# Performance work log

Measured on AMD Instinct MI355X. Metric: run time of the kernel, lower is better.

The kernel has to match this reference:

```python
import jax, jax.numpy as jnp
import numpy as np

N, C, H, W, J = 16, 8, 512, 1024, 8


def setup_inputs() -> dict:
    key = jax.random.key(0)
    logits = jax.random.normal(key, (N, C, H, W), dtype=jnp.float32)
    rng = np.random.default_rng(0)
    start = rng.integers(0, H - 2, size=(N, J))
    length = rng.integers(1, H // 2, size=(N, J))
    end = np.minimum(start + length, H - 1)          # ensure z+1 <= H-1
    ch = rng.integers(0, C, size=(N, J))
    params = jnp.asarray(np.stack([start, end, ch], axis=-1).astype(np.int32))
    return {"logits": logits, "params": params}


def reference(logits, params):
    n, c, h, w = logits.shape
    probs = jax.nn.softmax(logits, axis=-1)
    # soft-argmax expected position over grid axis -> [n, c, h]
    pos = jnp.sum(probs * jnp.arange(w, dtype=logits.dtype), axis=-1)
    # adjacent-row position differences -> [n, c, h-1]
    diff = pos[:, :, :-1] - pos[:, :, 1:]
    start = params[..., 0]   # [n, J]
    end = params[..., 1]     # [n, J]
    ch = params[..., 2]      # [n, J]
    # gather the channel for each (sample, lane): [n, J, h-1]
    diff_g = jnp.take_along_axis(diff, ch[:, :, None].astype(jnp.int32), axis=1)
    z = jnp.arange(h - 1, dtype=jnp.int32)
    mask = (z[None, None, :] >= start[:, :, None]) & (z[None, None, :] < end[:, :, None])
    # smooth_l1 vs zeros, mean over the ragged selected elements
    x = jnp.abs(diff_g)
    sl1 = jnp.where(x < 1.0, 0.5 * diff_g * diff_g, x - 0.5)
    mask_f = mask.astype(logits.dtype)
    total = jnp.sum(sl1 * mask_f)
    count = jnp.sum(mask_f)
    return total / count
```

## Files before the change

kernel.cpp:

```cpp
#include <hip/hip_runtime.h>

#define PN 16
#define PC 8
#define PH 512
#define PW 1024
#define PJ 8

#define NROWS (PN * PC * PH)
#define NWAVES 16384

__device__ __forceinline__ bool row_needed(const int* __restrict__ params, int row_id) {
    const int n = row_id >> 12;
    const int c = (row_id >> 9) & (PC - 1);
    const int h = row_id & (PH - 1);
    const int* pp = params + n * PJ * 3;
    bool needed = false;
#pragma unroll
    for (int j = 0; j < PJ; ++j) {
        const int s = pp[j * 3 + 0];
        const int e = pp[j * 3 + 1];
        const int ch = pp[j * 3 + 2];
        needed |= (ch == c) & (h >= s) & (h <= e);
    }
    return needed;
}

__global__ __launch_bounds__(256) void pos_kernel(const float* __restrict__ logits,
                                                  const int* __restrict__ params,
                                                  float* __restrict__ pos) {
    const int gwave = (blockIdx.x * blockDim.x + threadIdx.x) >> 6;
    const int lane = threadIdx.x & 63;

#pragma unroll
    for (int half = 0; half < 2; ++half) {
        const int r0 = 2 * gwave + half * 2 * NWAVES;
        const int r1 = r0 + 1;

        const bool needA = row_needed(params, r0);
        const bool needB = row_needed(params, r1);
        if (!(needA | needB)) continue;

        const float* rowA = logits + (size_t)r0 * PW;
        const float* rowB = logits + (size_t)r1 * PW;

        float4 a[4], b[4];
        if (needA) {
#pragma unroll
            for (int q = 0; q < 4; ++q)
                a[q] = *reinterpret_cast<const float4*>(rowA + q * 256 + lane * 4);
        }
        if (needB) {
#pragma unroll
            for (int q = 0; q < 4; ++q)
                b[q] = *reinterpret_cast<const float4*>(rowB + q * 256 + lane * 4);
        }

        if (needA) {
            float s = 0.f, sw = 0.f;
#pragma unroll
            for (int q = 0; q < 4; ++q) {
                const float base = (float)(q * 256 + lane * 4);
                float e0 = __expf(a[q].x);
                float e1 = __expf(a[q].y);
                float e2 = __expf(a[q].z);
                float e3 = __expf(a[q].w);
                s += e0 + e1 + e2 + e3;
                sw += e0 * base + e1 * (base + 1.f) + e2 * (base + 2.f) + e3 * (base + 3.f);
            }
#pragma unroll
            for (int off = 32; off > 0; off >>= 1) {
                s += __shfl_xor(s, off);
                sw += __shfl_xor(sw, off);
            }
            if (lane == 0) pos[r0] = sw / s;
        }
        if (needB) {
            float s = 0.f, sw = 0.f;
#pragma unroll
            for (int q = 0; q < 4; ++q) {
                const float base = (float)(q * 256 + lane * 4);
                float e0 = __expf(b[q].x);
                float e1 = __expf(b[q].y);
                float e2 = __expf(b[q].z);
                float e3 = __expf(b[q].w);
                s += e0 + e1 + e2 + e3;
                sw += e0 * base + e1 * (base + 1.f) + e2 * (base + 2.f) + e3 * (base + 3.f);
            }
#pragma unroll
            for (int off = 32; off > 0; off >>= 1) {
                s += __shfl_xor(s, off);
                sw += __shfl_xor(sw, off);
            }
            if (lane == 0) pos[r1] = sw / s;
        }
    }
}

__global__ __launch_bounds__(64) void loss_kernel(const float* __restrict__ pos,
                                                  const int* __restrict__ params,
                                                  float* __restrict__ partial) {
    const int nj = blockIdx.x;
    const int start = params[nj * 3 + 0];
    const int end   = params[nj * 3 + 1];
    const int ch    = params[nj * 3 + 2];

    const float* p = pos + ((size_t)(nj >> 3) * PC + ch) * PH;

    float sum = 0.f, cnt = 0.f;
    for (int z = start + (int)threadIdx.x; z < end; z += 64) {
        float d = p[z] - p[z + 1];
        float x = fabsf(d);
        sum += (x < 1.f) ? 0.5f * d * d : (x - 0.5f);
        cnt += 1.f;
    }
#pragma unroll
    for (int off = 32; off > 0; off >>= 1) {
        sum += __shfl_xor(sum, off);
        cnt += __shfl_xor(cnt, off);
    }
    if (threadIdx.x == 0) {
        partial[nj * 2 + 0] = sum;
        partial[nj * 2 + 1] = cnt;
    }
}

__global__ __launch_bounds__(64) void finalize_kernel(const float* __restrict__ partial,
                                                      float* __restrict__ out) {
    const int t = threadIdx.x;
    float s = partial[t * 2 + 0] + partial[(t + 64) * 2 + 0];
    float c = partial[t * 2 + 1] + partial[(t + 64) * 2 + 1];
#pragma unroll
    for (int off = 32; off > 0; off >>= 1) {
        s += __shfl_xor(s, off);
        c += __shfl_xor(c, off);
    }
    if (t == 0) out[0] = s / c;
}

extern "C" void kernel_launch(void* const* d_in, const int* in_sizes, int n_in,
                              void* d_out, int out_size, void* d_ws, size_t ws_size,
                              hipStream_t stream) {
    const float* logits = (const float*)d_in[0];
    const int* params = (const int*)d_in[1];
    float* out = (float*)d_out;

    float* pos = (float*)d_ws;
    float* partial = pos + NROWS;

    pos_kernel<<<NWAVES / 4, 256, 0, stream>>>(logits, params, pos);
    loss_kernel<<<PN * PJ, 64, 0, stream>>>(pos, params, partial);
    finalize_kernel<<<1, 64, 0, stream>>>(partial, out);
}
```

Measured before the change: 22.44 us.

## Compact needed rows via prefix-sum over interval params instead of per-row predicate

Instead of each wave testing a fixed pair of rows against all intervals and mostly idling, waves now map to a compacted list of needed rows built by walking the 128 (sample, lane) intervals with a running cumulative length. Waves with no assigned row exit early, so the work concentrates in the first few thousand waves and loads become denser. Each thread now loops over all 128 params serially, which adds scalar work. Rows covered by overlapping intervals are computed more than once, with the same value written to pos.

```diff
diff --git a/kernel.cpp b/kernel.cpp
--- a/kernel.cpp
+++ b/kernel.cpp
@@ -8,22 +8,7 @@
 
 #define NROWS (PN * PC * PH)
 #define NWAVES 16384
-
-__device__ __forceinline__ bool row_needed(const int* __restrict__ params, int row_id) {
-    const int n = row_id >> 12;
-    const int c = (row_id >> 9) & (PC - 1);
-    const int h = row_id & (PH - 1);
-    const int* pp = params + n * PJ * 3;
-    bool needed = false;
-#pragma unroll
-    for (int j = 0; j < PJ; ++j) {
-        const int s = pp[j * 3 + 0];
-        const int e = pp[j * 3 + 1];
-        const int ch = pp[j * 3 + 2];
-        needed |= (ch == c) & (h >= s) & (h <= e);
-    }
-    return needed;
-}
+#define NPAIRS (PN * PJ)
 
 __global__ __launch_bounds__(256) void pos_kernel(const float* __restrict__ logits,
                                                   const int* __restrict__ params,
@@ -31,68 +16,74 @@
     const int gwave = (blockIdx.x * blockDim.x + threadIdx.x) >> 6;
     const int lane = threadIdx.x & 63;
 
+    const int g0 = gwave;
+    const int g1 = gwave + NWAVES;
+
+    int row0 = -1, row1 = -1;
+    int cum = 0;
+    for (int p = 0; p < NPAIRS; ++p) {
+        const int s = params[p * 3 + 0];
+        const int e = params[p * 3 + 1];
+        const int ch = params[p * 3 + 2];
+        const int len = e - s + 1;
+        const int base = ((p >> 3) * PC + ch) * PH + s;
+        if (g0 >= cum && g0 < cum + len) row0 = base + (g0 - cum);
+        if (g1 >= cum && g1 < cum + len) row1 = base + (g1 - cum);
+        cum += len;
+    }
+    if ((row0 | row1) < 0 && row0 < 0 && row1 < 0) return;
+
+    float4 a[4], b[4];
+    if (row0 >= 0) {
+        const float* r = logits + (size_t)row0 * PW;
 #pragma unroll
-    for (int half = 0; half < 2; ++half) {
-        const int r0 = 2 * gwave + half * 2 * NWAVES;
-        const int r1 = r0 + 1;
+        for (int q = 0; q < 4; ++q)
+            a[q] = *reinterpret_cast<const float4*>(r + q * 256 + lane * 4);
+    }
+    if (row1 >= 0) {
+        const float* r = logits + (size_t)row1 * PW;
+#pragma unroll
+        for (int q = 0; q < 4; ++q)
+            b[q] = *reinterpret_cast<const float4*>(r + q * 256 + lane * 4);
+    }
 
-        const bool needA = row_needed(params, r0);
-        const bool needB = row_needed(params, r1);
-        if (!(needA | needB)) continue;
-
-        const float* rowA = logits + (size_t)r0 * PW;
-        const float* rowB = logits + (size_t)r1 * PW;
-
-        float4 a[4], b[4];
-        if (needA) {
+    if (row0 >= 0) {
+        float s = 0.f, sw = 0.f;
 #pragma unroll
-            for (int q = 0; q < 4; ++q)
-                a[q] = *reinterpret_cast<const float4*>(rowA + q * 256 + lane * 4);
+        for (int q = 0; q < 4; ++q) {
+            const float base = (float)(q * 256 + lane * 4);
+            float e0 = __expf(a[q].x);
+            float e1 = __expf(a[q].y);
+            float e2 = __expf(a[q].z);
+            float e3 = __expf(a[q].w);
+            s += e0 + e1 + e2 + e3;
+            sw += e0 * base + e1 * (base + 1.f) + e2 * (base + 2.f) + e3 * (base + 3.f);
         }
-        if (needB) {
 #pragma unroll
-            for (int q = 0; q < 4; ++q)
-                b[q] = *reinterpret_cast<const float4*>(rowB + q * 256 + lane * 4);
+        for (int off = 32; off > 0; off >>= 1) {
+            s += __shfl_xor(s, off);
+            sw += __shfl_xor(sw, off);
         }
-
-        if (needA) {
-            float s = 0.f, sw = 0.f;
+        if (lane == 0) pos[row0] = sw / s;
+    }
+    if (row1 >= 0) {
+        float s = 0.f, sw = 0.f;
 #pragma unroll
-            for (int q = 0; q < 4; ++q) {
-                const float base = (float)(q * 256 + lane * 4);
-                float e0 = __expf(a[q].x);
-                float e1 = __expf(a[q].y);
-                float e2 = __expf(a[q].z);
-                float e3 = __expf(a[q].w);
-                s += e0 + e1 + e2 + e3;
-                sw += e0 * base + e1 * (base + 1.f) + e2 * (base + 2.f) + e3 * (base + 3.f);
-            }
+        for (int q = 0; q < 4; ++q) {
+            const float base = (float)(q * 256 + lane * 4);
+            float e0 = __expf(b[q].x);
+            float e1 = __expf(b[q].y);
+            float e2 = __expf(b[q].z);
+            float e3 = __expf(b[q].w);
+            s += e0 + e1 + e2 + e3;
+            sw += e0 * base + e1 * (base + 1.f) + e2 * (base + 2.f) + e3 * (base + 3.f);
+        }
 #pragma unroll
-            for (int off = 32; off > 0; off >>= 1) {
-                s += __shfl_xor(s, off);
-                sw += __shfl_xor(sw, off);
-            }
-            if (lane == 0) pos[r0] = sw / s;
+        for (int off = 32; off > 0; off >>= 1) {
+            s += __shfl_xor(s, off);
+            sw += __shfl_xor(sw, off);
         }
-        if (needB) {
-            float s = 0.f, sw = 0.f;
-#pragma unroll
-            for (int q = 0; q < 4; ++q) {
-                const float base = (float)(q * 256 + lane * 4);
-                float e0 = __expf(b[q].x);
-                float e1 = __expf(b[q].y);
-                float e2 = __expf(b[q].z);
-                float e3 = __expf(b[q].w);
-                s += e0 + e1 + e2 + e3;
-                sw += e0 * base + e1 * (base + 1.f) + e2 * (base + 2.f) + e3 * (base + 3.f);
-            }
-#pragma unroll
-            for (int off = 32; off > 0; off >>= 1) {
-                s += __shfl_xor(s, off);
-                sw += __shfl_xor(sw, off);
-            }
-            if (lane == 0) pos[r1] = sw / s;
-        }
+        if (lane == 0) pos[row1] = sw / s;
     }
 }
 
```

Result: slower. 57.19 us (+154.9%).
